# Performance work log

Measured on AMD Instinct MI355X. Metric: run time of the kernel, lower is better.

The kernel has to match this reference:

```python
import jax, jax.numpy as jnp
import numpy as np

DIM = 768
NUM_HEADS = 12
HEAD_DIM = DIM // NUM_HEADS
SCALE = HEAD_DIM ** -0.5


def setup_inputs() -> dict:
    key = jax.random.key(0)
    ks = jax.random.split(key, 9)
    B, N = 2, 4096
    s = DIM ** -0.5
    return {
        "query": jax.random.normal(ks[0], (B, N, DIM), jnp.float32),
        "key": jax.random.normal(ks[1], (B, N, DIM), jnp.float32),
        "value": jax.random.normal(ks[2], (B, N, DIM), jnp.float32),
        "Wq": jax.random.normal(ks[3], (DIM, DIM), jnp.float32) * s,
        "Wk": jax.random.normal(ks[4], (DIM, DIM), jnp.float32) * s,
        "bk": jax.random.normal(ks[5], (DIM,), jnp.float32) * 0.02,
        "Wv": jax.random.normal(ks[6], (DIM, DIM), jnp.float32) * s,
        "Wp": jax.random.normal(ks[7], (DIM, DIM), jnp.float32) * s,
        "bp": jax.random.normal(ks[8], (DIM,), jnp.float32) * 0.02,
    }


def reference(query, key, value, Wq, Wk, bk, Wv, Wp, bp):
    B, Nq, C = query.shape
    Nk = key.shape[1]
    H, D = NUM_HEADS, HEAD_DIM
    # QKV projections (qv_bias=False -> no bias on q, v; k has bias)
    q = (query @ Wq.T).reshape(B, Nq, H, D).transpose(0, 2, 1, 3)  # [B,H,Nq,D]
    k = (key @ Wk.T + bk).reshape(B, Nk, H, D).transpose(0, 2, 1, 3)
    v = (value @ Wv.T).reshape(B, Nk, H, D).transpose(0, 2, 1, 3)
    # non-standard: exact GELU applied to K before QK^T
    k = jax.nn.gelu(k, approximate=False)
    attn = jnp.einsum("bhqd,bhkd->bhqk", q, k) * SCALE
    attn = jax.nn.softmax(attn, axis=-1)
    x = jnp.einsum("bhqk,bhkd->bhqd", attn, v)
    x = x.transpose(0, 2, 1, 3).reshape(B, Nq, C)
    return x @ Wp.T + bp
```

## Files before the change

kernel.cpp:

```cpp
#include <hip/hip_runtime.h>
#include <hip/hip_bf16.h>


#define DIM 768
#define NH 12
#define HD 64
#define NTOK 4096
#define WELEM 589824u
#define TELEM 6291456u

typedef short bf16x8 __attribute__((ext_vector_type(8)));
typedef float floatx4 __attribute__((ext_vector_type(4)));
typedef unsigned short us4 __attribute__((ext_vector_type(4)));

__device__ __forceinline__ float bf2f(unsigned short u) {
    union { unsigned int i; float f; } v; v.i = ((unsigned int)u) << 16; return v.f;
}
__device__ __forceinline__ unsigned short f2bf(float f) {
    union { float f; unsigned int i; } v; v.f = f;
    unsigned int r = v.i + 0x7fffu + ((v.i >> 16) & 1u);
    return (unsigned short)(r >> 16);
}
__device__ __forceinline__ unsigned int packbf(float a, float b) {
    __hip_bfloat162 h = __float22bfloat162_rn(make_float2(a, b));
    union { __hip_bfloat162 h; unsigned int u; } cv; cv.h = h; return cv.u;
}
__device__ __forceinline__ void gl2lds16(const unsigned short* g, unsigned short* l) {
    __builtin_amdgcn_global_load_lds(
        (const __attribute__((address_space(1))) unsigned int*)g,
        (__attribute__((address_space(3))) unsigned int*)l, 16, 0, 0);
}
__device__ __forceinline__ bf16x8 ld8_f32_to_bf16(const float* p) {
    floatx4 f0 = *(const floatx4*)p;
    floatx4 f1 = *(const floatx4*)(p + 4);
    union { unsigned int u[4]; bf16x8 v; } o;
    o.u[0] = packbf(f0[0], f0[1]);
    o.u[1] = packbf(f0[2], f0[3]);
    o.u[2] = packbf(f1[0], f1[1]);
    o.u[3] = packbf(f1[2], f1[3]);
    return o.v;
}

#if __has_builtin(__builtin_amdgcn_exp2f)
#define EXPFN(x) __builtin_amdgcn_exp2f(x)
#define QSCALE 0.18033688011f
#else
#define EXPFN(x) __expf(x)
#define QSCALE 0.125f
#endif

__global__ __launch_bounds__(256) void cvt_w(
    const float* __restrict__ a, const float* __restrict__ b,
    const float* __restrict__ c, const float* __restrict__ d,
    unsigned short* __restrict__ dst)
{
    size_t i = ((size_t)blockIdx.x * 256 + threadIdx.x) * 8;
    const float* s; size_t off;
    if (i < WELEM)            { s = a; off = i; }
    else if (i < 2u * WELEM)  { s = b; off = i - WELEM; }
    else if (i < 3u * WELEM)  { s = c; off = i - 2u * WELEM; }
    else                      { s = d; off = i - 3u * WELEM; }
    *(bf16x8*)(dst + i) = ld8_f32_to_bf16(s + off);
}

__global__ __launch_bounds__(256) void cvt_in(
    const float* __restrict__ a, const float* __restrict__ b,
    const float* __restrict__ c, unsigned short* __restrict__ dst)
{
    size_t i = ((size_t)blockIdx.x * 256 + threadIdx.x) * 8;
    const float* s; size_t off;
    if (i < TELEM)            { s = a; off = i; }
    else if (i < 2u * TELEM)  { s = b; off = i - TELEM; }
    else                      { s = c; off = i - 2u * TELEM; }
    *(bf16x8*)(dst + i) = ld8_f32_to_bf16(s + off);
}

template <int A_IS_BF16>
__device__ __forceinline__ void stage_tile(
    const void* __restrict__ Av, const unsigned short* __restrict__ W,
    unsigned short* Asb, unsigned short* Bsb,
    int m0, int n0, int k0, int w, int ro, int c, int cswz)
{
#pragma unroll
    for (int q = 0; q < 4; q++) {
        int rbase = w * 32 + q * 8;
        if (A_IS_BF16) {
            gl2lds16((const unsigned short*)Av + (size_t)(m0 + rbase + ro) * DIM + k0 + cswz,
                     Asb + rbase * 64);
        } else {
            bf16x8 a = ld8_f32_to_bf16((const float*)Av + (size_t)(m0 + rbase + ro) * DIM + k0 + c * 8);
            *(bf16x8*)(Asb + (rbase + ro) * 64 + cswz) = a;
        }
        gl2lds16(W + (size_t)(n0 + rbase + ro) * DIM + k0 + cswz, Bsb + rbase * 64);
    }
}

template <int A_IS_BF16>
__device__ __forceinline__ void gemm128(
    const void* __restrict__ Av, const unsigned short* __restrict__ W,
    const float* __restrict__ bias, void* __restrict__ Cv,
    int has_bias, int do_gelu, int trans, int out_f32)
{
    __shared__ unsigned short As[2][128 * 64];
    __shared__ unsigned short Bs[2][128 * 64];
    const int m0 = blockIdx.x * 128, n0 = blockIdx.y * 128;
    const int tid = threadIdx.x;
    const int w = tid >> 6, l = tid & 63;
    const int g = l >> 4, r16 = l & 15;
    const int wm = w >> 1, wn = w & 1;
    const int ro = l >> 3, c = l & 7;
    const int cswz = ((c ^ ro) & 7) * 8;
    const int NKT = DIM / 64;

    floatx4 acc[4][4];
#pragma unroll
    for (int i = 0; i < 4; i++)
#pragma unroll
        for (int j = 0; j < 4; j++) acc[i][j] = (floatx4){0.f, 0.f, 0.f, 0.f};

    stage_tile<A_IS_BF16>(Av, W, As[0], Bs[0], m0, n0, 0, w, ro, c, cswz);
    __syncthreads();

    for (int kt = 0; kt < NKT; kt++) {
        const int cur = kt & 1;

        if (kt + 1 < NKT)
            stage_tile<A_IS_BF16>(Av, W, As[cur ^ 1], Bs[cur ^ 1],
                                  m0, n0, (kt + 1) * 64, w, ro, c, cswz);

#pragma unroll
        for (int kk = 0; kk < 2; kk++) {
            bf16x8 af[4], bfr[4];
            int x = r16 & 7;
#pragma unroll
            for (int i = 0; i < 4; i++)
                af[i] = *(const bf16x8*)(As[cur] + (wm * 64 + i * 16 + r16) * 64 + (((kk * 4 + g) ^ x) * 8));
#pragma unroll
            for (int j = 0; j < 4; j++)
                bfr[j] = *(const bf16x8*)(Bs[cur] + (wn * 64 + j * 16 + r16) * 64 + (((kk * 4 + g) ^ x) * 8));
#pragma unroll
            for (int i = 0; i < 4; i++)
#pragma unroll
                for (int j = 0; j < 4; j++)
                    acc[i][j] = __builtin_amdgcn_mfma_f32_16x16x32_bf16(af[i], bfr[j], acc[i][j], 0, 0, 0);
        }
        __syncthreads();
    }

    if (trans) {
        unsigned short* C = (unsigned short*)Cv;
#pragma unroll
        for (int i = 0; i < 4; i++) {
            int m = m0 + wm * 64 + i * 16 + g * 4;
            int b = m >> 12, tloc = m & 4095;
#pragma unroll
            for (int j = 0; j < 4; j++) {
                int n = n0 + wn * 64 + j * 16 + r16;
                int h = n >> 6, d = n & 63;
                union { unsigned int u[2]; us4 v; } pk;
                pk.u[0] = packbf(acc[i][j][0], acc[i][j][1]);
                pk.u[1] = packbf(acc[i][j][2], acc[i][j][3]);
                *(us4*)(C + ((size_t)(b * NH + h) * 64 + d) * NTOK + tloc) = pk.v;
            }
        }
    } else {
#pragma unroll
        for (int i = 0; i < 4; i++)
#pragma unroll
            for (int j = 0; j < 4; j++) {
                int n = n0 + wn * 64 + j * 16 + r16;
                float bv = has_bias ? bias[n] : 0.f;
#pragma unroll
                for (int r = 0; r < 4; r++) {
                    int m = m0 + wm * 64 + i * 16 + g * 4 + r;
                    float v = acc[i][j][r] + bv;
                    if (do_gelu) v = 0.5f * v * (1.f + erff(v * 0.70710678118f));
                    if (out_f32) ((float*)Cv)[(size_t)m * DIM + n] = v;
                    else ((unsigned short*)Cv)[(size_t)m * DIM + n] = f2bf(v);
                }
            }
    }
}

template <int A_IS_BF16>
__global__ __launch_bounds__(256) void qkv_gemm(
    const void* __restrict__ q_in, const void* __restrict__ k_in,
    const void* __restrict__ v_in,
    const unsigned short* __restrict__ Wq, const unsigned short* __restrict__ Wk,
    const unsigned short* __restrict__ Wv, const float* __restrict__ bk,
    unsigned short* __restrict__ Qo, unsigned short* __restrict__ Ko,
    unsigned short* __restrict__ Vto)
{
    int z = blockIdx.z;
    const void* A = (z == 0) ? q_in : (z == 1) ? k_in : v_in;
    const unsigned short* W = (z == 0) ? Wq : (z == 1) ? Wk : Wv;
    unsigned short* C = (z == 0) ? Qo : (z == 1) ? Ko : Vto;
    gemm128<A_IS_BF16>(A, W, bk, C, z == 1, z == 1, z == 2, 0);
}

__global__ __launch_bounds__(256) void out_gemm(
    const unsigned short* __restrict__ X, const unsigned short* __restrict__ Wp,
    const float* __restrict__ bp, float* __restrict__ out)
{
    gemm128<1>(X, Wp, bp, out, 1, 0, 0, 1);
}

__device__ __forceinline__ int swzf(int R) { return (R & 7) ^ ((R >> 2) & 6); }

__global__ __launch_bounds__(256, 3) void attn_kernel(
    const unsigned short* __restrict__ Q, const unsigned short* __restrict__ K,
    const unsigned short* __restrict__ Vt, unsigned short* __restrict__ X)
{
    __shared__ unsigned short Ks[2][64 * 64];
    __shared__ unsigned short Vs[2][64 * 64];
    const int qt = blockIdx.x, bh = blockIdx.y;
    const int b = bh / NH, h = bh % NH;
    const int tid = threadIdx.x;
    const int w = tid >> 6, l = tid & 63;
    const int g = l >> 4, r16 = l & 15;
    const int tokbase = b * NTOK;

    bf16x8 qfr[2][2];
#pragma unroll
    for (int qfi = 0; qfi < 2; qfi++) {
        int qrow = tokbase + qt * 128 + w * 32 + qfi * 16 + r16;
#pragma unroll
        for (int kk = 0; kk < 2; kk++) {
            bf16x8 t = *(const bf16x8*)(Q + (size_t)qrow * DIM + h * HD + kk * 32 + g * 8);
#pragma unroll
            for (int j = 0; j < 8; j++)
                t[j] = (short)f2bf(bf2f((unsigned short)t[j]) * QSCALE);
            qfr[qfi][kk] = t;
        }
    }

    int koff[4][2], voff[4][2];
#pragma unroll
    for (int ct = 0; ct < 4; ct++) {
        int krow = (ct >> 1) * 32 + (r16 >> 2) * 8 + (ct & 1) * 4 + (r16 & 3);
#pragma unroll
        for (int kk = 0; kk < 2; kk++)
            koff[ct][kk] = krow * 64 + (((kk * 4 + g) ^ swzf(krow)) * 8);
    }
#pragma unroll
    for (int dt = 0; dt < 4; dt++) {
        int vrow = dt * 16 + r16;
#pragma unroll
        for (int c = 0; c < 2; c++)
            voff[dt][c] = vrow * 64 + (((c * 4 + g) ^ swzf(vrow)) * 8);
    }

    const int kv = w >> 1, half = w & 1;
    int soff[4];
    const int srl = l >> 3, scc = l & 7;
    const int sstride = (kv == 0) ? DIM : NTOK;
#pragma unroll
    for (int i = 0; i < 4; i++) {
        int row = half * 32 + i * 8 + srl;
        soff[i] = row * sstride + ((scc ^ swzf(row)) * 8);
    }
    const unsigned short* Kbase = K + (size_t)tokbase * DIM + h * HD;
    const unsigned short* Vbase = Vt + (size_t)bh * 64 * NTOK;

    floatx4 o[2][4];
#pragma unroll
    for (int qfi = 0; qfi < 2; qfi++)
#pragma unroll
        for (int dt = 0; dt < 4; dt++) o[qfi][dt] = (floatx4){0.f, 0.f, 0.f, 0.f};
    float lsum[2] = {0.f, 0.f};

    {
        const unsigned short* p = (kv == 0) ? Kbase : Vbase;
        unsigned short* dst = ((kv == 0) ? Ks[0] : Vs[0]) + half * 2048;
#pragma unroll
        for (int i = 0; i < 4; i++) gl2lds16(p + soff[i], dst + i * 512);
    }

    for (int kt = 0; kt < NTOK / 64; kt++) {
        const int cur = kt & 1;
        __syncthreads();

        bf16x8 kr[4][2], vr[4][2];
#pragma unroll
        for (int ct = 0; ct < 4; ct++)
#pragma unroll
            for (int kk = 0; kk < 2; kk++)
                kr[ct][kk] = *(const bf16x8*)(Ks[cur] + koff[ct][kk]);
#pragma unroll
        for (int dt = 0; dt < 4; dt++)
#pragma unroll
            for (int c = 0; c < 2; c++)
                vr[dt][c] = *(const bf16x8*)(Vs[cur] + voff[dt][c]);

        if (kt + 1 < NTOK / 64) {
            int keyg = (kt + 1) * 64;
            const unsigned short* p = (kv == 0) ? (Kbase + (size_t)keyg * DIM)
                                                : (Vbase + keyg);
            unsigned short* dst = ((kv == 0) ? Ks[cur ^ 1] : Vs[cur ^ 1]) + half * 2048;
#pragma unroll
            for (int i = 0; i < 4; i++) gl2lds16(p + soff[i], dst + i * 512);
        }

#pragma unroll
        for (int qfi = 0; qfi < 2; qfi++) {
            floatx4 s[4];
#pragma unroll
            for (int ct = 0; ct < 4; ct++) {
                floatx4 zz = (floatx4){0.f, 0.f, 0.f, 0.f};
                zz = __builtin_amdgcn_mfma_f32_16x16x32_bf16(kr[ct][0], qfr[qfi][0], zz, 0, 0, 0);
                s[ct] = __builtin_amdgcn_mfma_f32_16x16x32_bf16(kr[ct][1], qfr[qfi][1], zz, 0, 0, 0);
            }
            float ls0 = 0.f, ls1 = 0.f, ls2 = 0.f, ls3 = 0.f;
#pragma unroll
            for (int ct = 0; ct < 4; ct++) {
                float p0 = EXPFN(s[ct][0]);
                float p1 = EXPFN(s[ct][1]);
                float p2 = EXPFN(s[ct][2]);
                float p3 = EXPFN(s[ct][3]);
                s[ct][0] = p0; s[ct][1] = p1; s[ct][2] = p2; s[ct][3] = p3;
                ls0 += p0; ls1 += p1; ls2 += p2; ls3 += p3;
            }
            lsum[qfi] += (ls0 + ls1) + (ls2 + ls3);

            unsigned int pk[4][2];
#pragma unroll
            for (int ct = 0; ct < 4; ct++) {
                pk[ct][0] = packbf(s[ct][0], s[ct][1]);
                pk[ct][1] = packbf(s[ct][2], s[ct][3]);
            }
#pragma unroll
            for (int c = 0; c < 2; c++) {
                union { unsigned int u[4]; bf16x8 v; } bf;
                bf.u[0] = pk[2 * c][0]; bf.u[1] = pk[2 * c][1];
                bf.u[2] = pk[2 * c + 1][0]; bf.u[3] = pk[2 * c + 1][1];
#pragma unroll
                for (int dt = 0; dt < 4; dt++)
                    o[qfi][dt] = __builtin_amdgcn_mfma_f32_16x16x32_bf16(vr[dt][c], bf.v, o[qfi][dt], 0, 0, 0);
            }
        }
    }

#pragma unroll
    for (int qfi = 0; qfi < 2; qfi++) {
        lsum[qfi] += __shfl_xor(lsum[qfi], 16, 64);
        lsum[qfi] += __shfl_xor(lsum[qfi], 32, 64);
    }

#pragma unroll
    for (int qfi = 0; qfi < 2; qfi++) {
        float inv = 1.f / lsum[qfi];
        int tok = tokbase + qt * 128 + w * 32 + qfi * 16 + r16;
#pragma unroll
        for (int dt = 0; dt < 4; dt++) {
            union { unsigned int u[2]; us4 v; } pkv;
            pkv.u[0] = packbf(o[qfi][dt][0] * inv, o[qfi][dt][1] * inv);
            pkv.u[1] = packbf(o[qfi][dt][2] * inv, o[qfi][dt][3] * inv);
            *(us4*)(X + (size_t)tok * DIM + h * HD + dt * 16 + g * 4) = pkv.v;
        }
    }
}

extern "C" void kernel_launch(void* const* d_in, const int* in_sizes, int n_in,
                              void* d_out, int out_size, void* d_ws, size_t ws_size,
                              hipStream_t stream) {
    const float* query = (const float*)d_in[0];
    const float* key   = (const float*)d_in[1];
    const float* value = (const float*)d_in[2];
    const float* Wq    = (const float*)d_in[3];
    const float* Wk    = (const float*)d_in[4];
    const float* bk    = (const float*)d_in[5];
    const float* Wv    = (const float*)d_in[6];
    const float* Wp    = (const float*)d_in[7];
    const float* bp    = (const float*)d_in[8];
    float* out = (float*)d_out;

    unsigned short* ws = (unsigned short*)d_ws;
    unsigned short* Wqb = ws;
    unsigned short* Wkb = Wqb + WELEM;
    unsigned short* Wvb = Wkb + WELEM;
    unsigned short* Wpb = Wvb + WELEM;
    unsigned short* Qp  = Wpb + WELEM;
    unsigned short* Kp  = Qp + TELEM;
    unsigned short* Vtp = Kp + TELEM;
    unsigned short* Xp  = Vtp + TELEM;
    unsigned short* Qbf = Xp + TELEM;
    unsigned short* Kbf = Qbf + TELEM;
    unsigned short* Vbf = Kbf + TELEM;

    const size_t base_b = ((size_t)4 * WELEM + 4 * TELEM) * 2;
    const size_t cvt_b  = (size_t)3 * TELEM * 2;
    const bool cvt_ok = ws_size >= base_b + cvt_b;

    cvt_w<<<dim3(4 * WELEM / 8 / 256), 256, 0, stream>>>(Wq, Wk, Wv, Wp, Wqb);
    if (cvt_ok) {
        cvt_in<<<dim3(3 * TELEM / 8 / 256), 256, 0, stream>>>(query, key, value, Qbf);
        qkv_gemm<1><<<dim3(64, 6, 3), 256, 0, stream>>>(Qbf, Kbf, Vbf, Wqb, Wkb, Wvb, bk, Qp, Kp, Vtp);
    } else {
        qkv_gemm<0><<<dim3(64, 6, 3), 256, 0, stream>>>(query, key, value, Wqb, Wkb, Wvb, bk, Qp, Kp, Vtp);
    }
    attn_kernel<<<dim3(32, 24), 256, 0, stream>>>(Qp, Kp, Vtp, Xp);
    out_gemm<<<dim3(64, 6), 256, 0, stream>>>(Xp, Wpb, bp, out);
}
```

Measured before the change: 328.2 us.

## Shrink GEMM K-tile to 32 with new LDS swizzle; add MFMA priority hints in attention

The projection GEMM now stages K-tiles of 32 instead of 64, halving LDS use per buffer. It uses a new XOR swizzle, and the fragment offsets are precomputed outside the loop. This could raise occupancy and cut address arithmetic, at the cost of twice as many barriers and a shorter prefetch window. Separately, the attention loop wraps its MFMA sections in s_setprio raises so waves issuing matrix work get scheduling priority over waves doing exp/pack work.

```diff
diff --git a/kernel.cpp b/kernel.cpp
--- a/kernel.cpp
+++ b/kernel.cpp
@@ -76,22 +76,26 @@
 }
 
 template <int A_IS_BF16>
-__device__ __forceinline__ void stage_tile(
+__device__ __forceinline__ void stage32(
     const void* __restrict__ Av, const unsigned short* __restrict__ W,
     unsigned short* Asb, unsigned short* Bsb,
-    int m0, int n0, int k0, int w, int ro, int c, int cswz)
-{
-#pragma unroll
-    for (int q = 0; q < 4; q++) {
-        int rbase = w * 32 + q * 8;
+    int m0, int n0, int k0, int w, int l)
+{
+    const int ro = l >> 2;
+    const int gs = l & 3;
+#pragma unroll
+    for (int q = 0; q < 2; q++) {
+        int rbase = w * 32 + q * 16;
+        int row = rbase + ro;
+        int col = ((gs ^ ((row >> 1) & 3)) * 8);
         if (A_IS_BF16) {
-            gl2lds16((const unsigned short*)Av + (size_t)(m0 + rbase + ro) * DIM + k0 + cswz,
-                     Asb + rbase * 64);
+            gl2lds16((const unsigned short*)Av + (size_t)(m0 + row) * DIM + k0 + col,
+                     Asb + rbase * 32);
         } else {
-            bf16x8 a = ld8_f32_to_bf16((const float*)Av + (size_t)(m0 + rbase + ro) * DIM + k0 + c * 8);
-            *(bf16x8*)(Asb + (rbase + ro) * 64 + cswz) = a;
-        }
-        gl2lds16(W + (size_t)(n0 + rbase + ro) * DIM + k0 + cswz, Bsb + rbase * 64);
+            bf16x8 a = ld8_f32_to_bf16((const float*)Av + (size_t)(m0 + row) * DIM + k0 + col);
+            *(bf16x8*)(Asb + row * 32 + gs * 8) = a;
+        }
+        gl2lds16(W + (size_t)(n0 + row) * DIM + k0 + col, Bsb + rbase * 32);
     }
 }
 
@@ -101,16 +105,26 @@
     const float* __restrict__ bias, void* __restrict__ Cv,
     int has_bias, int do_gelu, int trans, int out_f32)
 {
-    __shared__ unsigned short As[2][128 * 64];
-    __shared__ unsigned short Bs[2][128 * 64];
+    __shared__ unsigned short As[2][128 * 32];
+    __shared__ unsigned short Bs[2][128 * 32];
     const int m0 = blockIdx.x * 128, n0 = blockIdx.y * 128;
     const int tid = threadIdx.x;
     const int w = tid >> 6, l = tid & 63;
     const int g = l >> 4, r16 = l & 15;
     const int wm = w >> 1, wn = w & 1;
-    const int ro = l >> 3, c = l & 7;
-    const int cswz = ((c ^ ro) & 7) * 8;
-    const int NKT = DIM / 64;
+    const int NKT = DIM / 32;
+
+    int aoff[4], boff[4];
+#pragma unroll
+    for (int i = 0; i < 4; i++) {
+        int row = wm * 64 + i * 16 + r16;
+        aoff[i] = row * 32 + ((g ^ ((row >> 1) & 3)) * 8);
+    }
+#pragma unroll
+    for (int j = 0; j < 4; j++) {
+        int row = wn * 64 + j * 16 + r16;
+        boff[j] = row * 32 + ((g ^ ((row >> 1) & 3)) * 8);
+    }
 
     floatx4 acc[4][4];
 #pragma unroll
@@ -118,32 +132,29 @@
 #pragma unroll
         for (int j = 0; j < 4; j++) acc[i][j] = (floatx4){0.f, 0.f, 0.f, 0.f};
 
-    stage_tile<A_IS_BF16>(Av, W, As[0], Bs[0], m0, n0, 0, w, ro, c, cswz);
+    stage32<A_IS_BF16>(Av, W, As[0], Bs[0], m0, n0, 0, w, l);
     __syncthreads();
 
     for (int kt = 0; kt < NKT; kt++) {
         const int cur = kt & 1;
 
         if (kt + 1 < NKT)
-            stage_tile<A_IS_BF16>(Av, W, As[cur ^ 1], Bs[cur ^ 1],
-                                  m0, n0, (kt + 1) * 64, w, ro, c, cswz);
-
-#pragma unroll
-        for (int kk = 0; kk < 2; kk++) {
-            bf16x8 af[4], bfr[4];
-            int x = r16 & 7;
-#pragma unroll
-            for (int i = 0; i < 4; i++)
-                af[i] = *(const bf16x8*)(As[cur] + (wm * 64 + i * 16 + r16) * 64 + (((kk * 4 + g) ^ x) * 8));
+            stage32<A_IS_BF16>(Av, W, As[cur ^ 1], Bs[cur ^ 1],
+                               m0, n0, (kt + 1) * 32, w, l);
+
+        bf16x8 af[4], bfr[4];
+#pragma unroll
+        for (int i = 0; i < 4; i++)
+            af[i] = *(const bf16x8*)(As[cur] + aoff[i]);
+#pragma unroll
+        for (int j = 0; j < 4; j++)
+            bfr[j] = *(const bf16x8*)(Bs[cur] + boff[j]);
+#pragma unroll
+        for (int i = 0; i < 4; i++)
 #pragma unroll
             for (int j = 0; j < 4; j++)
-                bfr[j] = *(const bf16x8*)(Bs[cur] + (wn * 64 + j * 16 + r16) * 64 + (((kk * 4 + g) ^ x) * 8));
-#pragma unroll
-            for (int i = 0; i < 4; i++)
-#pragma unroll
-                for (int j = 0; j < 4; j++)
-                    acc[i][j] = __builtin_amdgcn_mfma_f32_16x16x32_bf16(af[i], bfr[j], acc[i][j], 0, 0, 0);
-        }
+                acc[i][j] = __builtin_amdgcn_mfma_f32_16x16x32_bf16(af[i], bfr[j], acc[i][j], 0, 0, 0);
+
         __syncthreads();
     }
 
@@ -304,12 +315,14 @@
 #pragma unroll
         for (int qfi = 0; qfi < 2; qfi++) {
             floatx4 s[4];
+            __builtin_amdgcn_s_setprio(1);
 #pragma unroll
             for (int ct = 0; ct < 4; ct++) {
                 floatx4 zz = (floatx4){0.f, 0.f, 0.f, 0.f};
                 zz = __builtin_amdgcn_mfma_f32_16x16x32_bf16(kr[ct][0], qfr[qfi][0], zz, 0, 0, 0);
                 s[ct] = __builtin_amdgcn_mfma_f32_16x16x32_bf16(kr[ct][1], qfr[qfi][1], zz, 0, 0, 0);
             }
+            __builtin_amdgcn_s_setprio(0);
             float ls0 = 0.f, ls1 = 0.f, ls2 = 0.f, ls3 = 0.f;
 #pragma unroll
             for (int ct = 0; ct < 4; ct++) {
@@ -328,6 +341,7 @@
                 pk[ct][0] = packbf(s[ct][0], s[ct][1]);
                 pk[ct][1] = packbf(s[ct][2], s[ct][3]);
             }
+            __builtin_amdgcn_s_setprio(1);
 #pragma unroll
             for (int c = 0; c < 2; c++) {
                 union { unsigned int u[4]; bf16x8 v; } bf;
@@ -337,6 +351,7 @@
                 for (int dt = 0; dt < 4; dt++)
                     o[qfi][dt] = __builtin_amdgcn_mfma_f32_16x16x32_bf16(vr[dt][c], bf.v, o[qfi][dt], 0, 0, 0);
             }
+            __builtin_amdgcn_s_setprio(0);
         }
     }
 
```

After: 347.5 us. 5.9% more time.
